# Kernel tuning notes

Hardware: AMD Instinct MI355X
Metric: run time of the kernel (lower is better)

## Reference

```python
import jax, jax.numpy as jnp
import numpy as np

N, CH_IN, H, W = 4, 96, 128, 256
SF = 4  # scale_factor


def _conv(x, w, b):
    # 3x3 conv, stride 1, padding 1 ('SAME'), NCHW/OIHW layout
    y = jax.lax.conv_general_dilated(x, w, (1, 1), 'SAME',
                                     dimension_numbers=('NCHW', 'OIHW', 'NCHW'))
    return y + b[None, :, None, None]


def setup_inputs() -> dict:
    key = jax.random.key(0)
    ks = jax.random.split(key, 6)
    flow = jax.random.normal(ks[0], (N, 2, H, W), dtype=jnp.float32)
    feat = jax.random.normal(ks[1], (N, CH_IN, H, W), dtype=jnp.float32)
    # conv1: ch_in -> 128, conv2: 128 -> sf^2 * 9 = 144
    w1 = jax.random.normal(ks[2], (128, CH_IN, 3, 3), dtype=jnp.float32) * 0.05
    b1 = jax.random.normal(ks[3], (128,), dtype=jnp.float32) * 0.05
    w2 = jax.random.normal(ks[4], (SF * SF * 9, 128, 3, 3), dtype=jnp.float32) * 0.05
    b2 = jax.random.normal(ks[5], (SF * SF * 9,), dtype=jnp.float32) * 0.05
    return {'flow': flow, 'feat': feat, 'w1': w1, 'b1': b1, 'w2': w2, 'b2': b2}


def reference(flow, feat, w1, b1, w2, b2):
    n, _, h, w = flow.shape
    # convs: conv+LeakyReLU(0.1), then plain conv; mask scaled by 0.25
    hfeat = jax.nn.leaky_relu(_conv(feat, w1, b1), negative_slope=0.1)
    mask = 0.25 * _conv(hfeat, w2, b2)                      # (N, 144, H, W)
    # softmax over the 9 kernel positions
    m = mask.reshape(n, 9, SF, SF, h, w)                    # (N,9,4,4,H,W)
    m = jax.nn.softmax(m, axis=1)
    # unfold(4*flow, [3,3], padding=1): 9 shifted copies, row-major (ki,kj)
    fp = jnp.pad(4.0 * flow, ((0, 0), (0, 0), (1, 1), (1, 1)))
    patches = jnp.stack([fp[:, :, i:i + h, j:j + w]
                         for i in range(3) for j in range(3)], axis=2)  # (N,2,9,H,W)
    # convex combination over the 9 neighbors
    up = jnp.einsum('nkabhw,nckhw->ncabhw', m, patches)     # (N,2,4,4,H,W)
    up = up.transpose(0, 1, 4, 2, 5, 3)                     # (N,2,H,4,W,4)
    return up.reshape(n, 2, SF * h, SF * w)
```

## Files before the change

### kernel.cpp

```cpp
#include <hip/hip_runtime.h>
#include <hip/hip_bf16.h>

#define NN  4
#define CIN 96
#define C1  128
#define C2  144
#define HH  128
#define WW  256
#define NPX ((size_t)NN * HH * WW)

typedef short bf16x8 __attribute__((ext_vector_type(8)));
typedef float f32x4  __attribute__((ext_vector_type(4)));
typedef unsigned int u32x4 __attribute__((ext_vector_type(4)));

__device__ __forceinline__ short f2bs(float v) {
    __hip_bfloat16 b = __float2bfloat16(v);
    short s; __builtin_memcpy(&s, &b, 2); return s;
}

__device__ __forceinline__ void gld16(const void* g, void* l) {
    __builtin_amdgcn_global_load_lds(
        (const __attribute__((address_space(1))) void*)g,
        (__attribute__((address_space(3))) void*)l, 16, 0, 0);
}

__global__ __launch_bounds__(256) void transpose_feat(
    const float* __restrict__ feat, short* __restrict__ featT,
    short* __restrict__ zbuf)
{
    __shared__ unsigned int lds[48 * 258];
    const int tid = threadIdx.x;
    const int h = blockIdx.x & (HH - 1);
    const int n = blockIdx.x >> 7;

    if (blockIdx.x == 0 && tid < 32) zbuf[tid] = 0;

    #pragma unroll 4
    for (int cp = 0; cp < 48; ++cp) {
        float v0 = feat[(((size_t)n * CIN + 2 * cp    ) * HH + h) * WW + tid];
        float v1 = feat[(((size_t)n * CIN + 2 * cp + 1) * HH + h) * WW + tid];
        unsigned int p = (unsigned int)(unsigned short)f2bs(v0)
                       | ((unsigned int)(unsigned short)f2bs(v1) << 16);
        lds[cp * 258 + tid] = p;
    }
    __syncthreads();
    const size_t rowbase = (size_t)(n * HH + h) * WW * 32;
    #pragma unroll
    for (int kc = 0; kc < 3; ++kc) {
        short* dst = featT + (size_t)kc * (NPX * 32) + rowbase;
        #pragma unroll
        for (int it = 0; it < 4; ++it) {
            const int slot = it * 256 + tid;
            const int px = slot >> 2, sub = slot & 3;
            u32x4 v;
            #pragma unroll
            for (int k = 0; k < 4; ++k)
                v[k] = lds[(kc * 16 + sub * 4 + k) * 258 + px];
            *(u32x4*)&dst[(size_t)slot * 8] = v;
        }
    }
}

__global__ __launch_bounds__(256) void pack_wB(
    const float* __restrict__ w, short* __restrict__ wp,
    int cin, int nct, int total)
{
    int i = blockIdx.x * 256 + threadIdx.x;
    if (i >= total) return;
    const int j    = i & 7;
    const int col  = (i >> 3) & 15;
    const int quad = (i >> 7) & 3;
    int t = i >> 9;
    const int ct  = t % nct;  t /= nct;
    const int tap = t % 9;
    const int kci = t / 9;
    const int co = ct * 16 + col;
    const int ci = kci * 32 + quad * 8 + j;
    wp[i] = f2bs(w[((size_t)co * cin + ci) * 9 + tap]);
}

__global__ __launch_bounds__(256, 2) void conv1_mfma(
    const short* __restrict__ featT, const short* __restrict__ w1p,
    const float* __restrict__ b1, short* __restrict__ hfeat,
    const short* __restrict__ zbuf)
{
    __shared__ __attribute__((aligned(16))) short ldsA[3 * 258 * 32];
    __shared__ __attribute__((aligned(16))) short ldsB[3 * 8 * 512];
    const int tid  = threadIdx.x;
    const int bid  = ((blockIdx.x & 7) << 6) + (blockIdx.x >> 3);
    const int h    = bid & (HH - 1);
    const int n    = bid >> 7;
    const int lane = tid & 63, wave = tid >> 6;
    const int quad = lane >> 4, col = lane & 15;
    const int wp0  = wave * 64;

    f32x4 acc[4][8];
    #pragma unroll
    for (int mt = 0; mt < 4; ++mt)
        #pragma unroll
        for (int ct = 0; ct < 8; ++ct)
            #pragma unroll
            for (int r = 0; r < 4; ++r) acc[mt][ct][r] = 0.f;

    auto stageA = [&](int kci) {
        const short* cbase = featT + (size_t)kci * (NPX * 32);
        for (int s = tid; s < 3 * 258 * 4; s += 256) {
            const int cig = s & 3;
            const int px  = (s >> 2) % 258;
            const int row = (s >> 2) / 258;
            const int hh = h + row - 1, gw = px - 1;
            const short* g = zbuf;
            if (hh >= 0 && hh < HH && gw >= 0 && gw < WW)
                g = cbase + ((size_t)(n * HH + hh) * WW + gw) * 32
                    + ((cig ^ ((px >> 1) & 3)) << 3);
            gld16(g, &ldsA[s * 8]);
        }
    };
    auto stageB = [&](int kci, int tg) {
        const short* gB = w1p + (((size_t)(kci * 9 + tg * 3) * 8) << 9);
        for (int t = tid; t < 3 * 8 * 64; t += 256)
            gld16(gB + t * 8, &ldsB[t * 8]);
    };
    auto compute = [&](int tg) {
        #pragma unroll
        for (int dw = 0; dw < 3; ++dw) {
            bf16x8 af[4];
            #pragma unroll
            for (int mt = 0; mt < 4; ++mt) {
                const int px = wp0 + mt * 16 + col + dw;
                const int slot = (tg * 258 + px) * 4 + (quad ^ ((px >> 1) & 3));
                af[mt] = *(const bf16x8*)&ldsA[slot * 8];
            }
            #pragma unroll
            for (int ct = 0; ct < 8; ++ct) {
                const bf16x8 bfr = *(const bf16x8*)&ldsB[((dw * 8 + ct) << 9) + (lane << 3)];
                #pragma unroll
                for (int mt = 0; mt < 4; ++mt)
                    acc[mt][ct] = __builtin_amdgcn_mfma_f32_16x16x32_bf16(af[mt], bfr, acc[mt][ct], 0, 0, 0);
            }
        }
    };

    stageA(0);
    stageB(0, 0);
    __syncthreads();
    for (int kci = 0; kci < 3; ++kci)
        for (int tg = 0; tg < 3; ++tg) {
            compute(tg);
            __syncthreads();
            if (!(kci == 2 && tg == 2)) {
                int nk = kci, ntg = tg + 1;
                if (ntg == 3) { nk = kci + 1; ntg = 0; }
                if (ntg == 0) stageA(nk);
                stageB(nk, ntg);
                __syncthreads();
            }
        }

    float bias[8];
    #pragma unroll
    for (int ct = 0; ct < 8; ++ct) bias[ct] = b1[ct * 16 + col];
    #pragma unroll
    for (int mt = 0; mt < 4; ++mt)
        #pragma unroll
        for (int r = 0; r < 4; ++r) {
            const int w = wp0 + mt * 16 + quad * 4 + r;
            const size_t pxw = (size_t)(n * HH + h) * WW + w;
            #pragma unroll
            for (int ct = 0; ct < 8; ++ct) {
                float a = acc[mt][ct][r] + bias[ct];
                a = a > 0.f ? a : 0.1f * a;
                hfeat[((size_t)(ct >> 1) * NPX + pxw) * 32 + (ct & 1) * 16 + col] = f2bs(a);
            }
        }
}

__global__ __launch_bounds__(256, 2) void conv2_fused(
    const short* __restrict__ hfeat, const short* __restrict__ w2p,
    const float* __restrict__ b2, const float* __restrict__ flow,
    float* __restrict__ out, const short* __restrict__ zbuf)
{
    __shared__ __attribute__((aligned(16))) short ldsA[3 * 258 * 32];
    __shared__ __attribute__((aligned(16))) short ldsB[3 * 9 * 512];
    const int tid  = threadIdx.x;
    const int bid  = ((blockIdx.x & 7) << 6) + (blockIdx.x >> 3);
    const int h    = bid & (HH - 1);
    const int n    = bid >> 7;
    const int lane = tid & 63, wave = tid >> 6;
    const int quad = lane >> 4, col = lane & 15;
    const int wp0  = wave * 64;

    f32x4 acc[4][9];
    #pragma unroll
    for (int mt = 0; mt < 4; ++mt)
        #pragma unroll
        for (int ct = 0; ct < 9; ++ct)
            #pragma unroll
            for (int r = 0; r < 4; ++r) acc[mt][ct][r] = 0.f;

    auto stageA = [&](int kci) {
        const short* cbase = hfeat + (size_t)kci * (NPX * 32);
        for (int s = tid; s < 3 * 258 * 4; s += 256) {
            const int cig = s & 3;
            const int px  = (s >> 2) % 258;
            const int row = (s >> 2) / 258;
            const int hh = h + row - 1, gw = px - 1;
            const short* g = zbuf;
            if (hh >= 0 && hh < HH && gw >= 0 && gw < WW)
                g = cbase + ((size_t)(n * HH + hh) * WW + gw) * 32
                    + ((cig ^ ((px >> 1) & 3)) << 3);
            gld16(g, &ldsA[s * 8]);
        }
    };
    auto stageB = [&](int kci, int tg) {
        const short* gB = w2p + (((size_t)(kci * 9 + tg * 3) * 9) << 9);
        for (int t = tid; t < 3 * 9 * 64; t += 256)
            gld16(gB + t * 8, &ldsB[t * 8]);
    };
    auto compute = [&](int tg) {
        #pragma unroll
        for (int dw = 0; dw < 3; ++dw) {
            bf16x8 af[4];
            #pragma unroll
            for (int mt = 0; mt < 4; ++mt) {
                const int px = wp0 + mt * 16 + col + dw;
                const int slot = (tg * 258 + px) * 4 + (quad ^ ((px >> 1) & 3));
                af[mt] = *(const bf16x8*)&ldsA[slot * 8];
            }
            #pragma unroll
            for (int ct = 0; ct < 9; ++ct) {
                const bf16x8 bfr = *(const bf16x8*)&ldsB[((dw * 9 + ct) << 9) + (lane << 3)];
                #pragma unroll
                for (int mt = 0; mt < 4; ++mt)
                    acc[mt][ct] = __builtin_amdgcn_mfma_f32_16x16x32_bf16(af[mt], bfr, acc[mt][ct], 0, 0, 0);
            }
        }
    };

    stageA(0);
    stageB(0, 0);
    __syncthreads();
    for (int kci = 0; kci < 4; ++kci)
        for (int tg = 0; tg < 3; ++tg) {
            compute(tg);
            __syncthreads();
            if (!(kci == 3 && tg == 2)) {
                int nk = kci, ntg = tg + 1;
                if (ntg == 3) { nk = kci + 1; ntg = 0; }
                if (ntg == 0) stageA(nk);
                stageB(nk, ntg);
                __syncthreads();
            }
        }

    float* outs = (float*)ldsA;
    float* flds = (float*)ldsA + 8224;
    for (int i = tid; i < 2 * 3 * 258; i += 256) {
        const int px = i % 258;
        const int t  = i / 258;
        const int row = t % 3, c = t / 3;
        const int hh = h + row - 1, gw = px - 1;
        float v = 0.f;
        if (hh >= 0 && hh < HH && gw >= 0 && gw < WW)
            v = flow[(((size_t)n * 2 + c) * HH + hh) * WW + gw];
        flds[(c * 3 + row) * 264 + px] = v;
    }
    __syncthreads();

    const int a_ = col >> 2, b_ = col & 3;
    float bias[9];
    #pragma unroll
    for (int k = 0; k < 9; ++k) bias[k] = b2[k * 16 + col];

    #pragma unroll
    for (int mt = 0; mt < 4; ++mt) {
        const int w0 = wp0 + mt * 16 + quad * 4;
        float fw[2][3][6];
        #pragma unroll
        for (int c = 0; c < 2; ++c)
            #pragma unroll
            for (int ki = 0; ki < 3; ++ki)
                #pragma unroll
                for (int j = 0; j < 6; ++j)
                    fw[c][ki][j] = flds[(c * 3 + ki) * 264 + w0 + j];
        #pragma unroll
        for (int r = 0; r < 4; ++r) {
            const int w = w0 + r;
            float v[9], mx = -1e30f;
            #pragma unroll
            for (int k = 0; k < 9; ++k) {
                v[k] = 0.25f * (acc[mt][k][r] + bias[k]);
                mx = fmaxf(mx, v[k]);
            }
            float s = 0.f;
            #pragma unroll
            for (int k = 0; k < 9; ++k) { v[k] = __expf(v[k] - mx); s += v[k]; }
            const float inv = 4.f / s;
            float o0 = 0.f, o1 = 0.f;
            #pragma unroll
            for (int ki = 0; ki < 3; ++ki)
                #pragma unroll
                for (int kj = 0; kj < 3; ++kj) {
                    const float wgt = v[ki * 3 + kj];
                    o0 += wgt * fw[0][ki][r + kj];
                    o1 += wgt * fw[1][ki][r + kj];
                }
            outs[(0 * 4 + a_) * 1028 + 4 * w + b_] = o0 * inv;
            outs[(1 * 4 + a_) * 1028 + 4 * w + b_] = o1 * inv;
        }
    }
    __syncthreads();

    const int H4 = 4 * HH, W4 = 4 * WW;
    #pragma unroll
    for (int it = 0; it < 32; ++it) {
        const int i = it * 256 + tid;
        const int w4 = i & 1023, a = (i >> 10) & 3, c = i >> 12;
        out[(((size_t)(n * 2 + c)) * H4 + 4 * h + a) * W4 + w4] =
            outs[(c * 4 + a) * 1028 + w4];
    }
}

extern "C" void kernel_launch(void* const* d_in, const int* in_sizes, int n_in,
                              void* d_out, int out_size, void* d_ws, size_t ws_size,
                              hipStream_t stream)
{
    const float* flow = (const float*)d_in[0];
    const float* feat = (const float*)d_in[1];
    const float* w1   = (const float*)d_in[2];
    const float* b1   = (const float*)d_in[3];
    const float* w2   = (const float*)d_in[4];
    const float* b2   = (const float*)d_in[5];
    float* out = (float*)d_out;

    short* featT = (short*)d_ws;
    short* hfeat = featT + (size_t)3 * NPX * 32;
    short* w1p   = hfeat + (size_t)4 * NPX * 32;
    short* w2p   = w1p + (size_t)3 * 9 * 8 * 512;
    short* zbuf  = w2p + (size_t)4 * 9 * 9 * 512;

    const int tot1 = 3 * 9 * 8 * 512;
    const int tot2 = 4 * 9 * 9 * 512;

    transpose_feat<<<NN * HH, 256, 0, stream>>>(feat, featT, zbuf);
    pack_wB<<<(tot1 + 255) / 256, 256, 0, stream>>>(w1, w1p, CIN, 8, tot1);
    pack_wB<<<(tot2 + 255) / 256, 256, 0, stream>>>(w2, w2p, C1, 9, tot2);
    conv1_mfma<<<NN * HH, 256, 0, stream>>>(featT, w1p, b1, hfeat, zbuf);
    conv2_fused<<<NN * HH, 256, 0, stream>>>(hfeat, w2p, b2, flow, out, zbuf);
}
```

Measured before the change: 177.0 us.

## Double-buffer per-tap weight tiles in both conv kernels

Both conv kernels now stage one tap's weight slice at a time into a two-slot LDS buffer and prefetch the next tap's weights while the current tap's MFMAs run. Previously a three-tap weight group was loaded with a barrier-separated stall before each compute step. The change overlaps weight loads with compute and drops one barrier per step, but adds more barriers per channel chunk (one per tap). The activation staging at each new channel chunk still stalls the pipeline with no overlap.

```diff
diff --git a/kernel.cpp b/kernel.cpp
--- a/kernel.cpp
+++ b/kernel.cpp
@@ -85,7 +85,7 @@
     const short* __restrict__ zbuf)
 {
     __shared__ __attribute__((aligned(16))) short ldsA[3 * 258 * 32];
-    __shared__ __attribute__((aligned(16))) short ldsB[3 * 8 * 512];
+    __shared__ __attribute__((aligned(16))) short ldsB[2][8 * 512];
     const int tid  = threadIdx.x;
     const int bid  = ((blockIdx.x & 7) << 6) + (blockIdx.x >> 3);
     const int h    = bid & (HH - 1);
@@ -116,46 +116,47 @@
             gld16(g, &ldsA[s * 8]);
         }
     };
-    auto stageB = [&](int kci, int tg) {
-        const short* gB = w1p + (((size_t)(kci * 9 + tg * 3) * 8) << 9);
-        for (int t = tid; t < 3 * 8 * 64; t += 256)
-            gld16(gB + t * 8, &ldsB[t * 8]);
-    };
-    auto compute = [&](int tg) {
-        #pragma unroll
-        for (int dw = 0; dw < 3; ++dw) {
-            bf16x8 af[4];
-            #pragma unroll
-            for (int mt = 0; mt < 4; ++mt) {
-                const int px = wp0 + mt * 16 + col + dw;
-                const int slot = (tg * 258 + px) * 4 + (quad ^ ((px >> 1) & 3));
-                af[mt] = *(const bf16x8*)&ldsA[slot * 8];
-            }
-            #pragma unroll
-            for (int ct = 0; ct < 8; ++ct) {
-                const bf16x8 bfr = *(const bf16x8*)&ldsB[((dw * 8 + ct) << 9) + (lane << 3)];
-                #pragma unroll
-                for (int mt = 0; mt < 4; ++mt)
-                    acc[mt][ct] = __builtin_amdgcn_mfma_f32_16x16x32_bf16(af[mt], bfr, acc[mt][ct], 0, 0, 0);
-            }
+    auto stageB = [&](int q, int pbuf) {
+        const short* gB = w1p + (((size_t)q * 8) << 9);
+        #pragma unroll
+        for (int t = 0; t < 2; ++t)
+            gld16(gB + (t * 256 + tid) * 8, &ldsB[pbuf][(t * 256 + tid) * 8]);
+    };
+    auto compute = [&](int tap, const short* Bbuf) {
+        const int dh = tap / 3, dw = tap % 3;
+        bf16x8 af[4];
+        #pragma unroll
+        for (int mt = 0; mt < 4; ++mt) {
+            const int px = wp0 + mt * 16 + col + dw;
+            const int slot = (dh * 258 + px) * 4 + (quad ^ ((px >> 1) & 3));
+            af[mt] = *(const bf16x8*)&ldsA[slot * 8];
+        }
+        #pragma unroll
+        for (int ct = 0; ct < 8; ++ct) {
+            const bf16x8 bfr = *(const bf16x8*)&Bbuf[(ct << 9) + (lane << 3)];
+            #pragma unroll
+            for (int mt = 0; mt < 4; ++mt)
+                acc[mt][ct] = __builtin_amdgcn_mfma_f32_16x16x32_bf16(af[mt], bfr, acc[mt][ct], 0, 0, 0);
         }
     };
 
     stageA(0);
     stageB(0, 0);
     __syncthreads();
-    for (int kci = 0; kci < 3; ++kci)
-        for (int tg = 0; tg < 3; ++tg) {
-            compute(tg);
+    int p = 0;
+    for (int kci = 0; kci < 3; ++kci) {
+        if (kci) {
+            stageA(kci);
             __syncthreads();
-            if (!(kci == 2 && tg == 2)) {
-                int nk = kci, ntg = tg + 1;
-                if (ntg == 3) { nk = kci + 1; ntg = 0; }
-                if (ntg == 0) stageA(nk);
-                stageB(nk, ntg);
-                __syncthreads();
-            }
-        }
+        }
+        for (int tap = 0; tap < 9; ++tap) {
+            const int q = kci * 9 + tap;
+            if (q < 26) stageB(q + 1, p ^ 1);
+            compute(tap, ldsB[p]);
+            __syncthreads();
+            p ^= 1;
+        }
+    }
 
     float bias[8];
     #pragma unroll
@@ -181,7 +182,7 @@
     float* __restrict__ out, const short* __restrict__ zbuf)
 {
     __shared__ __attribute__((aligned(16))) short ldsA[3 * 258 * 32];
-    __shared__ __attribute__((aligned(16))) short ldsB[3 * 9 * 512];
+    __shared__ __attribute__((aligned(16))) short ldsB[2][9 * 512];
     const int tid  = threadIdx.x;
     const int bid  = ((blockIdx.x & 7) << 6) + (blockIdx.x >> 3);
     const int h    = bid & (HH - 1);
@@ -212,46 +213,46 @@
             gld16(g, &ldsA[s * 8]);
         }
     };
-    auto stageB = [&](int kci, int tg) {
-        const short* gB = w2p + (((size_t)(kci * 9 + tg * 3) * 9) << 9);
-        for (int t = tid; t < 3 * 9 * 64; t += 256)
-            gld16(gB + t * 8, &ldsB[t * 8]);
-    };
-    auto compute = [&](int tg) {
-        #pragma unroll
-        for (int dw = 0; dw < 3; ++dw) {
-            bf16x8 af[4];
-            #pragma unroll
-            for (int mt = 0; mt < 4; ++mt) {
-                const int px = wp0 + mt * 16 + col + dw;
-                const int slot = (tg * 258 + px) * 4 + (quad ^ ((px >> 1) & 3));
-                af[mt] = *(const bf16x8*)&ldsA[slot * 8];
-            }
-            #pragma unroll
-            for (int ct = 0; ct < 9; ++ct) {
-                const bf16x8 bfr = *(const bf16x8*)&ldsB[((dw * 9 + ct) << 9) + (lane << 3)];
-                #pragma unroll
-                for (int mt = 0; mt < 4; ++mt)
-                    acc[mt][ct] = __builtin_amdgcn_mfma_f32_16x16x32_bf16(af[mt], bfr, acc[mt][ct], 0, 0, 0);
-            }
+    auto stageB = [&](int q, int pbuf) {
+        const short* gB = w2p + (((size_t)q * 9) << 9);
+        for (int t = tid; t < 576; t += 256)
+            gld16(gB + t * 8, &ldsB[pbuf][t * 8]);
+    };
+    auto compute = [&](int tap, const short* Bbuf) {
+        const int dh = tap / 3, dw = tap % 3;
+        bf16x8 af[4];
+        #pragma unroll
+        for (int mt = 0; mt < 4; ++mt) {
+            const int px = wp0 + mt * 16 + col + dw;
+            const int slot = (dh * 258 + px) * 4 + (quad ^ ((px >> 1) & 3));
+            af[mt] = *(const bf16x8*)&ldsA[slot * 8];
+        }
+        #pragma unroll
+        for (int ct = 0; ct < 9; ++ct) {
+            const bf16x8 bfr = *(const bf16x8*)&Bbuf[(ct << 9) + (lane << 3)];
+            #pragma unroll
+            for (int mt = 0; mt < 4; ++mt)
+                acc[mt][ct] = __builtin_amdgcn_mfma_f32_16x16x32_bf16(af[mt], bfr, acc[mt][ct], 0, 0, 0);
         }
     };
 
     stageA(0);
     stageB(0, 0);
     __syncthreads();
-    for (int kci = 0; kci < 4; ++kci)
-        for (int tg = 0; tg < 3; ++tg) {
-            compute(tg);
+    int p = 0;
+    for (int kci = 0; kci < 4; ++kci) {
+        if (kci) {
+            stageA(kci);
             __syncthreads();
-            if (!(kci == 3 && tg == 2)) {
-                int nk = kci, ntg = tg + 1;
-                if (ntg == 3) { nk = kci + 1; ntg = 0; }
-                if (ntg == 0) stageA(nk);
-                stageB(nk, ntg);
-                __syncthreads();
-            }
-        }
+        }
+        for (int tap = 0; tap < 9; ++tap) {
+            const int q = kci * 9 + tap;
+            if (q < 35) stageB(q + 1, p ^ 1);
+            compute(tap, ldsB[p]);
+            __syncthreads();
+            p ^= 1;
+        }
+    }
 
     float* outs = (float*)ldsA;
     float* flds = (float*)ldsA + 8224;
```

Result: slower. 181.4 us (+2.5%).
